# Kernel tuning notes

Hardware: AMD Instinct MI355X
Metric: run time of the kernel (lower is better)

Reference implementation:

```python
import jax, jax.numpy as jnp
import numpy as np

NUM_EMBEDDINGS = 8192
EMBEDDING_DIM = 64
COMMITMENT_COST = 0.25


def setup_inputs() -> dict:
    key = jax.random.key(0)
    k1, k2 = jax.random.split(key)
    hidden_states = jax.random.normal(k1, (32, 32, 32, EMBEDDING_DIM), dtype=jnp.float32)
    init_bound = 1.0 / NUM_EMBEDDINGS
    embedding = jax.random.uniform(k2, (NUM_EMBEDDINGS, EMBEDDING_DIM), dtype=jnp.float32,
                                   minval=-init_bound, maxval=init_bound)
    return {"hidden_states": hidden_states, "embedding": embedding}


def reference(hidden_states, embedding):
    # hidden_states: (B, H, W, D); embedding: (K, D)
    flat = hidden_states.reshape(-1, EMBEDDING_DIM)            # (N, D)
    z_sq = jnp.sum(flat * flat, axis=1, keepdims=True)          # (N, 1)
    e_sq = jnp.sum(embedding * embedding, axis=1)               # (K,)
    # squared L2 distances: ||z||^2 + ||e||^2 - 2 z.e
    distances = z_sq + e_sq - 2.0 * (flat @ embedding.T)        # (N, K)
    encoding_indices = jnp.argmin(distances, axis=1)            # (N,)
    # one-hot @ embedding == gather; identical math, efficient form
    quantized = jnp.take(embedding, encoding_indices, axis=0).reshape(hidden_states.shape)
    # codebook + commitment loss (return_loss=True path)
    loss = (jnp.mean((jax.lax.stop_gradient(quantized) - hidden_states) ** 2)
            + COMMITMENT_COST * jnp.mean((quantized - jax.lax.stop_gradient(hidden_states)) ** 2))
    # straight-through estimator
    z_q = hidden_states + jax.lax.stop_gradient(quantized - hidden_states)
    B = hidden_states.shape[0]
    min_encoding_indices = encoding_indices.reshape(B, -1)      # (B, num_tokens)
    return z_q, min_encoding_indices, loss
```

## Files before the change

### kernel.cpp

```cpp
#include <hip/hip_runtime.h>
#include <cfloat>

#define N_TOK   32768
#define DIM     64
#define K_CODES 8192
#define NCHK    64
#define TPB     128

#define IDX_OFF  (N_TOK * DIM)
#define LOSS_OFF (N_TOK * DIM + N_TOK)

#define WS_ESQ   0
#define WS_EHIT  8192
#define WS_PART  270336

#define W2_ESQ   0
#define W2_EHIT  8192
#define W2_ET    270336
#define W2_MM    794624
#define W2_PART  1843200
#define W2_TOTAL 1843456

#define MRG   2e-5f
#define DINIT 6e-5f

typedef __attribute__((ext_vector_type(8)))  short bf16x8;
typedef __attribute__((ext_vector_type(16))) float f32x16;

__device__ inline ushort f2bf(float x) {
    unsigned u = __float_as_uint(x);
    return (ushort)((u + 0x7FFFu + ((u >> 16) & 1u)) >> 16);
}
__device__ inline float bf2f(ushort h) { return __uint_as_float(((unsigned)h) << 16); }
__device__ inline ushort f2bf_up(float x) {
    unsigned u = __float_as_uint(x);
    return (x >= 0.0f) ? (ushort)((u + 0xFFFFu) >> 16) : (ushort)(u >> 16);
}
__device__ inline unsigned long long packdi(float d, int i) {
    unsigned u = __float_as_uint(d);
    u ^= (u & 0x80000000u) ? 0xFFFFFFFFu : 0x80000000u;
    return ((unsigned long long)u << 32) | (unsigned)i;
}

__global__ __launch_bounds__(256) void esq_kernel(const float* __restrict__ emb,
                                                  float* __restrict__ esq) {
#pragma clang fp contract(off)
    const int tid = threadIdx.x;
    const int q = tid & 7;
    const int code = blockIdx.x * 32 + (tid >> 3);
    const float* row = emb + code * DIM;
    float x = row[q];
    float r = x * x;
#pragma unroll
    for (int m = 1; m < 8; ++m) {
        float y = row[q + 8 * m];
        float sq = y * y;
        r = r + sq;
    }
    r = r + __shfl_xor(r, 1, 64);
    r = r + __shfl_xor(r, 2, 64);
    r = r + __shfl_xor(r, 4, 64);
    if (q == 0) esq[code] = r;
}

__global__ __launch_bounds__(256) void pack2(const float* __restrict__ emb,
                                             ushort* __restrict__ ehiT,
                                             float* __restrict__ eT) {
#pragma clang fp contract(off)
    const int k = blockIdx.x * 256 + threadIdx.x;
    float v[64];
    {
        const float4* ep = (const float4*)(emb + (size_t)k * DIM);
#pragma unroll
        for (int i = 0; i < 16; ++i) {
            const float4 a = ep[i];
            v[4 * i] = a.x; v[4 * i + 1] = a.y; v[4 * i + 2] = a.z; v[4 * i + 3] = a.w;
        }
    }
#pragma unroll
    for (int j = 0; j < 64; ++j) eT[(size_t)j * K_CODES + k] = v[j];
    const int sc = k >> 7, lc = k & 127;
#pragma unroll
    for (int q = 0; q < 4; ++q)
#pragma unroll
        for (int h = 0; h < 2; ++h) {
            bf16x8 o;
#pragma unroll
            for (int e = 0; e < 8; ++e) o[e] = (short)f2bf(v[16 * q + 8 * h + e]);
            *(bf16x8*)(ehiT + ((((size_t)sc * 4 + q) * 2 + h) * 128 + lc) * 8) = o;
        }
}

__global__ __launch_bounds__(256, 2) void vq_mfma(const float* __restrict__ hid,
                                                  const ushort* __restrict__ ehiT,
                                                  ushort* __restrict__ Mm) {
#pragma clang fp contract(off)
    const int tid = threadIdx.x;
    const int lane = tid & 63;
    const int w = tid >> 6;
    const int h = lane >> 5;
    const int t0 = blockIdx.x * 64;

    bf16x8 z_hi[2][4];
#pragma unroll
    for (int ts = 0; ts < 2; ++ts)
#pragma unroll
    for (int q = 0; q < 4; ++q) {
        const float* zp = hid + (size_t)(t0 + 32 * ts + (lane & 31)) * DIM + 16 * q + 8 * h;
        const float4 u0 = *(const float4*)zp;
        const float4 u1 = *(const float4*)(zp + 4);
        const float zz[8] = {u0.x, u0.y, u0.z, u0.w, u1.x, u1.y, u1.z, u1.w};
        bf16x8 hv;
#pragma unroll
        for (int i = 0; i < 8; ++i) hv[i] = (short)f2bf(zz[i]);
        z_hi[ts][q] = hv;
    }

    f32x16 zc;
#pragma unroll
    for (int i = 0; i < 16; ++i) zc[i] = 0.0f;

#define ALOAD(SC, R, Q) (*(const bf16x8*)(ehiT + \
    ((((size_t)(SC) * 4 + (Q)) * 2 + h) * 128 + 32 * (R) + (lane & 31)) * 8))

    bf16x8 Aa[4][4], Ab[4][4];
#pragma unroll
    for (int r = 0; r < 4; ++r)
#pragma unroll
        for (int q = 0; q < 4; ++q) Aa[r][q] = ALOAD(w, r, q);

#define MFMA_G(CUR, NXT, G) { \
    const int sc = 4 * (G) + w; \
    const int scn = ((G) + 1 < 16) ? (4 * ((G) + 1) + w) : sc; \
    _Pragma("unroll") \
    for (int r = 0; r < 4; ++r) \
        _Pragma("unroll") \
        for (int q = 0; q < 4; ++q) NXT[r][q] = ALOAD(scn, r, q); \
    float wm0 = -3.0e38f, wm1 = -3.0e38f; \
    _Pragma("unroll") \
    for (int r = 0; r < 4; ++r) { \
        f32x16 d0 = __builtin_amdgcn_mfma_f32_32x32x16_bf16(CUR[r][0], z_hi[0][0], zc, 0, 0, 0); \
        f32x16 d1 = __builtin_amdgcn_mfma_f32_32x32x16_bf16(CUR[r][0], z_hi[1][0], zc, 0, 0, 0); \
        _Pragma("unroll") \
        for (int q = 1; q < 4; ++q) { \
            d0 = __builtin_amdgcn_mfma_f32_32x32x16_bf16(CUR[r][q], z_hi[0][q], d0, 0, 0, 0); \
            d1 = __builtin_amdgcn_mfma_f32_32x32x16_bf16(CUR[r][q], z_hi[1][q], d1, 0, 0, 0); \
        } \
        _Pragma("unroll") \
        for (int i = 0; i < 16; ++i) { \
            wm0 = fmaxf(wm0, d0[i]); \
            wm1 = fmaxf(wm1, d1[i]); \
        } \
    } \
    wm0 = fmaxf(wm0, __shfl_xor(wm0, 32, 64)); \
    wm1 = fmaxf(wm1, __shfl_xor(wm1, 32, 64)); \
    if (lane < 32) { \
        Mm[(size_t)sc * N_TOK + t0 + lane]      = f2bf_up(wm0); \
        Mm[(size_t)sc * N_TOK + t0 + 32 + lane] = f2bf_up(wm1); \
    } }

    for (int gg = 0; gg < 16; gg += 2) {
        MFMA_G(Aa, Ab, gg)
        MFMA_G(Ab, Aa, gg + 1)
    }
#undef MFMA_G
#undef ALOAD
}

template <int FUSED>
__global__ __launch_bounds__(512, 1) void vq_select_t(const float* __restrict__ hid,
                                                      const float* __restrict__ eT,
                                                      const float* __restrict__ esq,
                                                      const ushort* __restrict__ Mm,
                                                      const float* __restrict__ emb,
                                                      float* __restrict__ out_zq,
                                                      float* __restrict__ out_idx,
                                                      float* __restrict__ partials) {
#pragma clang fp contract(off)
    __shared__ float z_s[TPB][68];
    __shared__ float zsq_s[TPB];
    __shared__ float eps_s[TPB];
    __shared__ float bD_s[TPB];
    __shared__ float mxw[4][TPB];
    __shared__ unsigned long long key_s[TPB];
    __shared__ unsigned long long m0_s[NCHK];
    __shared__ unsigned long long m1_s[NCHK];
    __shared__ float lred[2];

    const int tid = threadIdx.x;
    const int lane = tid & 63;
    const int w = tid >> 6;
    const int t0 = blockIdx.x * TPB;

    {
        const int t = tid >> 2;
        const int j4 = (tid & 3) * 4;
        const float4* src = (const float4*)(hid + (size_t)(t0 + t) * DIM);
        float4* dst = (float4*)(&z_s[t][0]);
#pragma unroll
        for (int i = 0; i < 4; ++i) dst[j4 + i] = src[j4 + i];
    }
    if (tid < TPB) key_s[tid] = ~0ull;
    __syncthreads();

    {
        const int token = tid & 127;
        const int cg = tid >> 7;
        float pm = bf2f(Mm[(size_t)(16 * cg) * N_TOK + t0 + token]);
#pragma unroll 5
        for (int c = 16 * cg + 1; c < 16 * cg + 16; ++c)
            pm = fmaxf(pm, bf2f(Mm[(size_t)c * N_TOK + t0 + token]));
        mxw[cg][token] = pm;
    }
    if (tid < TPB) {
        const float* zr = &z_s[tid][0];
        float r[8];
#pragma unroll
        for (int q = 0; q < 8; ++q) {
            float x = zr[q]; r[q] = x * x;
#pragma unroll
            for (int m = 1; m < 8; ++m) {
                float y = zr[q + 8 * m];
                float sq = y * y;
                r[q] = r[q] + sq;
            }
        }
        zsq_s[tid] = ((r[0] + r[1]) + (r[2] + r[3])) + ((r[4] + r[5]) + (r[6] + r[7]));
    }
    __syncthreads();
    if (tid < TPB) {
        const float mx = fmaxf(fmaxf(mxw[0][tid], mxw[1][tid]),
                               fmaxf(mxw[2][tid], mxw[3][tid]));
        const float zsq = zsq_s[tid];
        const float eps = sqrtf(zsq) * 4.2e-6f + 2e-7f;
        eps_s[tid] = eps;
        bD_s[tid] = zsq - 2.0f * mx + 2.0f * eps + DINIT;
    }
    __syncthreads();

#pragma unroll
    for (int i = 0; i < 8; ++i) {
        const int c = 8 * w + i;
        const float mA = bf2f(Mm[(size_t)c * N_TOK + t0 + lane]);
        const int sA = (fmaf(-2.0f, mA + eps_s[lane], zsq_s[lane]) - MRG) < bD_s[lane];
        const unsigned long long b0 = __ballot(sA);
        const float mB = bf2f(Mm[(size_t)c * N_TOK + t0 + 64 + lane]);
        const int sB = (fmaf(-2.0f, mB + eps_s[64 + lane], zsq_s[64 + lane]) - MRG) < bD_s[64 + lane];
        const unsigned long long b1 = __ballot(sB);
        if (lane == 0) { m0_s[c] = b0; m1_s[c] = b1; }
    }

    for (int i = 0; i < 8; ++i) {
        const int c = 8 * w + i;
        unsigned long long msk0 = m0_s[c], msk1 = m1_s[c];
        if (!(msk0 | msk1)) continue;
        const int k0 = c * 128 + 2 * lane;
        const float* eb = eT + k0;
        const float2 es2 = *(const float2*)(esq + k0);

        while (msk0 | msk1) {
            int G = 1;
            int tA, tB;
            if (msk0) { tA = __ffsll(msk0) - 1; msk0 &= msk0 - 1; }
            else      { tA = 64 + __ffsll(msk1) - 1; msk1 &= msk1 - 1; }
            tB = tA;
            if (msk0 | msk1) {
                G = 2;
                if (msk0) { tB = __ffsll(msk0) - 1; msk0 &= msk0 - 1; }
                else      { tB = 64 + __ffsll(msk1) - 1; msk1 &= msk1 - 1; }
            }
            const float4* zpA = (const float4*)(&z_s[tA][0]);
            const float4* zpB = (const float4*)(&z_s[tB][0]);

            float2 bA[8], bB[8];
            float aA0, aA1, aB0, aB1;
#define LOADG(B, G2) { _Pragma("unroll") \
    for (int j = 0; j < 8; ++j) \
        B[j] = *(const float2*)(eb + (size_t)(8 * (G2) + j) * K_CODES); }
#define FMAJ(Bj, vA, vB, COMP) \
    aA0 = fmaf(vA.COMP, Bj.x, aA0); aA1 = fmaf(vA.COMP, Bj.y, aA1); \
    aB0 = fmaf(vB.COMP, Bj.x, aB0); aB1 = fmaf(vB.COMP, Bj.y, aB1);
#define FMAG(B, G2) { \
    const float4 vA = zpA[2 * (G2)], vB = zpB[2 * (G2)]; \
    FMAJ(B[0], vA, vB, x) FMAJ(B[1], vA, vB, y) \
    FMAJ(B[2], vA, vB, z) FMAJ(B[3], vA, vB, w) \
    const float4 uA = zpA[2 * (G2) + 1], uB = zpB[2 * (G2) + 1]; \
    FMAJ(B[4], uA, uB, x) FMAJ(B[5], uA, uB, y) \
    FMAJ(B[6], uA, uB, z) FMAJ(B[7], uA, uB, w) }

            LOADG(bA, 0)
            LOADG(bB, 1)
            {
                const float4 vA = zpA[0], vB = zpB[0];
                aA0 = vA.x * bA[0].x; aA1 = vA.x * bA[0].y;
                aB0 = vB.x * bA[0].x; aB1 = vB.x * bA[0].y;
                FMAJ(bA[1], vA, vB, y)
                FMAJ(bA[2], vA, vB, z)
                FMAJ(bA[3], vA, vB, w)
                const float4 uA = zpA[1], uB = zpB[1];
                FMAJ(bA[4], uA, uB, x)
                FMAJ(bA[5], uA, uB, y)
                FMAJ(bA[6], uA, uB, z)
                FMAJ(bA[7], uA, uB, w)
            }
            LOADG(bA, 2) FMAG(bB, 1)
            LOADG(bB, 3) FMAG(bA, 2)
            LOADG(bA, 4) FMAG(bB, 3)
            LOADG(bB, 5) FMAG(bA, 4)
            LOADG(bA, 6) FMAG(bB, 5)
            LOADG(bB, 7) FMAG(bA, 6)
            FMAG(bB, 7)
#undef LOADG
#undef FMAJ
#undef FMAG

#define FINISH(aX0, aX1, tX) { \
    const float zqX = zsq_s[tX]; \
    const float dX0 = fmaf(-2.0f, aX0, zqX + es2.x); \
    const float dX1 = fmaf(-2.0f, aX1, zqX + es2.y); \
    float dl = dX0; int il = k0; \
    if (dX1 < dl) { dl = dX1; il = k0 + 1; } \
    _Pragma("unroll") \
    for (int mm = 1; mm < 64; mm <<= 1) { \
        const float ov = __shfl_xor(dl, mm, 64); \
        const int   oi = __shfl_xor(il, mm, 64); \
        if (ov < dl || (ov == dl && oi < il)) { dl = ov; il = oi; } \
    } \
    if (lane == 0) atomicMin(&key_s[tX], packdi(dl, il)); }

            FINISH(aA0, aA1, tA)
            if (G > 1) FINISH(aB0, aB1, tB)
#undef FINISH
        }
    }
    __syncthreads();

    if (FUSED) {
        if (tid < TPB) {
            const int t = t0 + tid;
            const int bi = (int)(key_s[tid] & 0xFFFFFFFFull);
            out_idx[t] = (float)bi;
            const float4* q4 = (const float4*)(emb + (size_t)bi * DIM);
            const float4* h4 = (const float4*)(&z_s[tid][0]);
            float4* o4 = (float4*)(out_zq + (size_t)t * DIM);
            float lsum = 0.f;
#pragma unroll
            for (int i = 0; i < 16; ++i) {
                const float4 q = q4[i];
                const float4 h = h4[i];
                float4 zq;
                float dx;
                dx = q.x - h.x; zq.x = h.x + dx; lsum += dx * dx;
                dx = q.y - h.y; zq.y = h.y + dx; lsum += dx * dx;
                dx = q.z - h.z; zq.z = h.z + dx; lsum += dx * dx;
                dx = q.w - h.w; zq.w = h.w + dx; lsum += dx * dx;
                o4[i] = zq;
            }
#pragma unroll
            for (int off = 32; off >= 1; off >>= 1) lsum += __shfl_xor(lsum, off, 64);
            if ((tid & 63) == 0) lred[tid >> 6] = lsum;
        }
        __syncthreads();
        if (tid == 0) partials[blockIdx.x] = lred[0] + lred[1];
    } else {
        if (tid < TPB) out_idx[t0 + tid] = (float)(int)(key_s[tid] & 0xFFFFFFFFull);
    }
}

__global__ __launch_bounds__(256) void vq_finish(const float* __restrict__ hid,
                                                 const float* __restrict__ emb,
                                                 const float* __restrict__ out_idx,
                                                 float* __restrict__ out_zq,
                                                 float* __restrict__ partials) {
#pragma clang fp contract(off)
    __shared__ float lred[4];
    const int tid = threadIdx.x;
    const int t = blockIdx.x * 256 + tid;

    const int bi = (int)out_idx[t];

    const float4* q4 = (const float4*)(emb + (size_t)bi * DIM);
    const float4* h4 = (const float4*)(hid + (size_t)t * DIM);
    float4* o4 = (float4*)(out_zq + (size_t)t * DIM);
    float lsum = 0.f;
#pragma unroll
    for (int i = 0; i < 16; ++i) {
        const float4 q = q4[i];
        const float4 h = h4[i];
        float4 zq;
        float dx;
        dx = q.x - h.x; zq.x = h.x + dx; lsum += dx * dx;
        dx = q.y - h.y; zq.y = h.y + dx; lsum += dx * dx;
        dx = q.z - h.z; zq.z = h.z + dx; lsum += dx * dx;
        dx = q.w - h.w; zq.w = h.w + dx; lsum += dx * dx;
        o4[i] = zq;
    }

#pragma unroll
    for (int off = 32; off >= 1; off >>= 1) lsum += __shfl_xor(lsum, off, 64);
    const int wid = tid >> 6;
    if ((tid & 63) == 0) lred[wid] = lsum;
    __syncthreads();
    if (tid == 0) partials[blockIdx.x] = (lred[0] + lred[1]) + (lred[2] + lred[3]);
}

__global__ __launch_bounds__(128) void loss_kernel128(const float* __restrict__ partials,
                                                      float* __restrict__ out_loss) {
#pragma clang fp contract(off)
    __shared__ float s[128];
    const int t = threadIdx.x;
    s[t] = partials[t];
    __syncthreads();
    for (int off = 64; off >= 1; off >>= 1) {
        if (t < off) s[t] = s[t] + s[t + off];
        __syncthreads();
    }
    if (t == 0) {
        const float m = s[0] * (1.0f / 2097152.0f);
        out_loss[0] = m + 0.25f * m;
    }
}

__global__ __launch_bounds__(128) void loss_kernel256(const float* __restrict__ partials,
                                                      float* __restrict__ out_loss) {
#pragma clang fp contract(off)
    __shared__ float s[128];
    const int t = threadIdx.x;
    s[t] = partials[t] + partials[t + 128];
    __syncthreads();
    for (int off = 64; off >= 1; off >>= 1) {
        if (t < off) s[t] = s[t] + s[t + off];
        __syncthreads();
    }
    if (t == 0) {
        const float m = s[0] * (1.0f / 2097152.0f);
        out_loss[0] = m + 0.25f * m;
    }
}

extern "C" void kernel_launch(void* const* d_in, const int* in_sizes, int n_in,
                              void* d_out, int out_size, void* d_ws, size_t ws_size,
                              hipStream_t stream) {
    const float* hid = (const float*)d_in[0];
    const float* emb = (const float*)d_in[1];
    float* out = (float*)d_out;
    float* ws  = (float*)d_ws;

    if (ws_size >= (size_t)W2_TOTAL * sizeof(float)) {
        float*  esq   = ws + W2_ESQ;
        ushort* ehiT  = (ushort*)(ws + W2_EHIT);
        float*  eT    = ws + W2_ET;
        ushort* Mm    = (ushort*)(ws + W2_MM);
        float*  parts = ws + W2_PART;

        esq_kernel<<<K_CODES / 32, 256, 0, stream>>>(emb, esq);
        pack2<<<K_CODES / 256, 256, 0, stream>>>(emb, ehiT, eT);
        vq_mfma<<<N_TOK / 64, 256, 0, stream>>>(hid, ehiT, Mm);
        vq_select_t<1><<<N_TOK / TPB, 512, 0, stream>>>(hid, eT, esq, Mm, emb,
                                                        out, out + IDX_OFF, parts);
        loss_kernel256<<<1, 128, 0, stream>>>(parts, out + LOSS_OFF);
    } else {
        float*  esq   = ws + WS_ESQ;
        ushort* ehiT  = (ushort*)(ws + WS_EHIT);
        float*  parts = ws + WS_PART;
        float*  eT    = out;
        ushort* Mm    = (ushort*)(out + 524288);

        esq_kernel<<<K_CODES / 32, 256, 0, stream>>>(emb, esq);
        pack2<<<K_CODES / 256, 256, 0, stream>>>(emb, ehiT, eT);
        vq_mfma<<<N_TOK / 64, 256, 0, stream>>>(hid, ehiT, Mm);
        vq_select_t<0><<<N_TOK / TPB, 512, 0, stream>>>(hid, eT, esq, Mm, emb,
                                                        out, out + IDX_OFF, parts);
        vq_finish<<<N_TOK / 256, 256, 0, stream>>>(hid, emb, out + IDX_OFF, out, parts);
        loss_kernel128<<<1, 128, 0, stream>>>(parts, out + LOSS_OFF);
    }
}
```

Baseline: 132.4 us.

## Evaluate best-bound chunk first to tighten pruning threshold before candidate scan

The select kernel now records which 128-code chunk has the highest bf16 upper-bound score per token and evaluates that chunk exactly first. The exact best distance found there replaces the heuristic bound (zsq - 2*max + slack) as the pruning threshold for the remaining chunks, so fewer chunks pass the filter and need exact FP32 dot products. It adds an extra pass with two more block barriers, and it serializes the first-chunk evaluation before the main scan.

```diff
diff --git a/kernel.cpp b/kernel.cpp
--- a/kernel.cpp
+++ b/kernel.cpp
@@ -22,7 +22,6 @@
 #define W2_TOTAL 1843456
 
 #define MRG   2e-5f
-#define DINIT 6e-5f
 
 typedef __attribute__((ext_vector_type(8)))  short bf16x8;
 typedef __attribute__((ext_vector_type(16))) float f32x16;
@@ -40,6 +39,11 @@
     unsigned u = __float_as_uint(d);
     u ^= (u & 0x80000000u) ? 0xFFFFFFFFu : 0x80000000u;
     return ((unsigned long long)u << 32) | (unsigned)i;
+}
+__device__ inline float unpackd(unsigned long long k) {
+    unsigned u = (unsigned)(k >> 32);
+    u = (u & 0x80000000u) ? (u ^ 0x80000000u) : ~u;
+    return __uint_as_float(u);
 }
 
 __global__ __launch_bounds__(256) void esq_kernel(const float* __restrict__ emb,
@@ -167,113 +171,37 @@
 #undef ALOAD
 }
 
-template <int FUSED>
-__global__ __launch_bounds__(512, 1) void vq_select_t(const float* __restrict__ hid,
-                                                      const float* __restrict__ eT,
-                                                      const float* __restrict__ esq,
-                                                      const ushort* __restrict__ Mm,
-                                                      const float* __restrict__ emb,
-                                                      float* __restrict__ out_zq,
-                                                      float* __restrict__ out_idx,
-                                                      float* __restrict__ partials) {
-#pragma clang fp contract(off)
-    __shared__ float z_s[TPB][68];
-    __shared__ float zsq_s[TPB];
-    __shared__ float eps_s[TPB];
-    __shared__ float bD_s[TPB];
-    __shared__ float mxw[4][TPB];
-    __shared__ unsigned long long key_s[TPB];
-    __shared__ unsigned long long m0_s[NCHK];
-    __shared__ unsigned long long m1_s[NCHK];
-    __shared__ float lred[2];
-
-    const int tid = threadIdx.x;
-    const int lane = tid & 63;
-    const int w = tid >> 6;
-    const int t0 = blockIdx.x * TPB;
-
-    {
-        const int t = tid >> 2;
-        const int j4 = (tid & 3) * 4;
-        const float4* src = (const float4*)(hid + (size_t)(t0 + t) * DIM);
-        float4* dst = (float4*)(&z_s[t][0]);
-#pragma unroll
-        for (int i = 0; i < 4; ++i) dst[j4 + i] = src[j4 + i];
-    }
-    if (tid < TPB) key_s[tid] = ~0ull;
-    __syncthreads();
-
-    {
-        const int token = tid & 127;
-        const int cg = tid >> 7;
-        float pm = bf2f(Mm[(size_t)(16 * cg) * N_TOK + t0 + token]);
-#pragma unroll 5
-        for (int c = 16 * cg + 1; c < 16 * cg + 16; ++c)
-            pm = fmaxf(pm, bf2f(Mm[(size_t)c * N_TOK + t0 + token]));
-        mxw[cg][token] = pm;
-    }
-    if (tid < TPB) {
-        const float* zr = &z_s[tid][0];
-        float r[8];
-#pragma unroll
-        for (int q = 0; q < 8; ++q) {
-            float x = zr[q]; r[q] = x * x;
-#pragma unroll
-            for (int m = 1; m < 8; ++m) {
-                float y = zr[q + 8 * m];
-                float sq = y * y;
-                r[q] = r[q] + sq;
-            }
-        }
-        zsq_s[tid] = ((r[0] + r[1]) + (r[2] + r[3])) + ((r[4] + r[5]) + (r[6] + r[7]));
-    }
-    __syncthreads();
-    if (tid < TPB) {
-        const float mx = fmaxf(fmaxf(mxw[0][tid], mxw[1][tid]),
-                               fmaxf(mxw[2][tid], mxw[3][tid]));
-        const float zsq = zsq_s[tid];
-        const float eps = sqrtf(zsq) * 4.2e-6f + 2e-7f;
-        eps_s[tid] = eps;
-        bD_s[tid] = zsq - 2.0f * mx + 2.0f * eps + DINIT;
-    }
-    __syncthreads();
-
-#pragma unroll
-    for (int i = 0; i < 8; ++i) {
-        const int c = 8 * w + i;
-        const float mA = bf2f(Mm[(size_t)c * N_TOK + t0 + lane]);
-        const int sA = (fmaf(-2.0f, mA + eps_s[lane], zsq_s[lane]) - MRG) < bD_s[lane];
-        const unsigned long long b0 = __ballot(sA);
-        const float mB = bf2f(Mm[(size_t)c * N_TOK + t0 + 64 + lane]);
-        const int sB = (fmaf(-2.0f, mB + eps_s[64 + lane], zsq_s[64 + lane]) - MRG) < bD_s[64 + lane];
-        const unsigned long long b1 = __ballot(sB);
-        if (lane == 0) { m0_s[c] = b0; m1_s[c] = b1; }
-    }
-
-    for (int i = 0; i < 8; ++i) {
-        const int c = 8 * w + i;
-        unsigned long long msk0 = m0_s[c], msk1 = m1_s[c];
-        if (!(msk0 | msk1)) continue;
-        const int k0 = c * 128 + 2 * lane;
-        const float* eb = eT + k0;
-        const float2 es2 = *(const float2*)(esq + k0);
-
-        while (msk0 | msk1) {
-            int G = 1;
-            int tA, tB;
-            if (msk0) { tA = __ffsll(msk0) - 1; msk0 &= msk0 - 1; }
-            else      { tA = 64 + __ffsll(msk1) - 1; msk1 &= msk1 - 1; }
-            tB = tA;
-            if (msk0 | msk1) {
-                G = 2;
-                if (msk0) { tB = __ffsll(msk0) - 1; msk0 &= msk0 - 1; }
-                else      { tB = 64 + __ffsll(msk1) - 1; msk1 &= msk1 - 1; }
-            }
-            const float4* zpA = (const float4*)(&z_s[tA][0]);
-            const float4* zpB = (const float4*)(&z_s[tB][0]);
-
-            float2 bA[8], bB[8];
-            float aA0, aA1, aB0, aB1;
+__device__ __forceinline__ void eval_chunk(const int c,
+                                           unsigned long long msk0,
+                                           unsigned long long msk1,
+                                           const float* __restrict__ eT,
+                                           const float* __restrict__ esq,
+                                           const float (*z_s)[68],
+                                           const float* zsq_s,
+                                           unsigned long long* key_s,
+                                           const int lane) {
+#pragma clang fp contract(off)
+    if (!(msk0 | msk1)) return;
+    const int k0 = c * 128 + 2 * lane;
+    const float* eb = eT + k0;
+    const float2 es2 = *(const float2*)(esq + k0);
+
+    while (msk0 | msk1) {
+        int G = 1;
+        int tA, tB;
+        if (msk0) { tA = __ffsll(msk0) - 1; msk0 &= msk0 - 1; }
+        else      { tA = 64 + __ffsll(msk1) - 1; msk1 &= msk1 - 1; }
+        tB = tA;
+        if (msk0 | msk1) {
+            G = 2;
+            if (msk0) { tB = __ffsll(msk0) - 1; msk0 &= msk0 - 1; }
+            else      { tB = 64 + __ffsll(msk1) - 1; msk1 &= msk1 - 1; }
+        }
+        const float4* zpA = (const float4*)(&z_s[tA][0]);
+        const float4* zpB = (const float4*)(&z_s[tB][0]);
+
+        float2 bA[8], bB[8];
+        float aA0, aA1, aB0, aB1;
 #define LOADG(B, G2) { _Pragma("unroll") \
     for (int j = 0; j < 8; ++j) \
         B[j] = *(const float2*)(eb + (size_t)(8 * (G2) + j) * K_CODES); }
@@ -288,28 +216,28 @@
     FMAJ(B[4], uA, uB, x) FMAJ(B[5], uA, uB, y) \
     FMAJ(B[6], uA, uB, z) FMAJ(B[7], uA, uB, w) }
 
-            LOADG(bA, 0)
-            LOADG(bB, 1)
-            {
-                const float4 vA = zpA[0], vB = zpB[0];
-                aA0 = vA.x * bA[0].x; aA1 = vA.x * bA[0].y;
-                aB0 = vB.x * bA[0].x; aB1 = vB.x * bA[0].y;
-                FMAJ(bA[1], vA, vB, y)
-                FMAJ(bA[2], vA, vB, z)
-                FMAJ(bA[3], vA, vB, w)
-                const float4 uA = zpA[1], uB = zpB[1];
-                FMAJ(bA[4], uA, uB, x)
-                FMAJ(bA[5], uA, uB, y)
-                FMAJ(bA[6], uA, uB, z)
-                FMAJ(bA[7], uA, uB, w)
-            }
-            LOADG(bA, 2) FMAG(bB, 1)
-            LOADG(bB, 3) FMAG(bA, 2)
-            LOADG(bA, 4) FMAG(bB, 3)
-            LOADG(bB, 5) FMAG(bA, 4)
-            LOADG(bA, 6) FMAG(bB, 5)
-            LOADG(bB, 7) FMAG(bA, 6)
-            FMAG(bB, 7)
+        LOADG(bA, 0)
+        LOADG(bB, 1)
+        {
+            const float4 vA = zpA[0], vB = zpB[0];
+            aA0 = vA.x * bA[0].x; aA1 = vA.x * bA[0].y;
+            aB0 = vB.x * bA[0].x; aB1 = vB.x * bA[0].y;
+            FMAJ(bA[1], vA, vB, y)
+            FMAJ(bA[2], vA, vB, z)
+            FMAJ(bA[3], vA, vB, w)
+            const float4 uA = zpA[1], uB = zpB[1];
+            FMAJ(bA[4], uA, uB, x)
+            FMAJ(bA[5], uA, uB, y)
+            FMAJ(bA[6], uA, uB, z)
+            FMAJ(bA[7], uA, uB, w)
+        }
+        LOADG(bA, 2) FMAG(bB, 1)
+        LOADG(bB, 3) FMAG(bA, 2)
+        LOADG(bA, 4) FMAG(bB, 3)
+        LOADG(bB, 5) FMAG(bA, 4)
+        LOADG(bA, 6) FMAG(bB, 5)
+        LOADG(bB, 7) FMAG(bA, 6)
+        FMAG(bB, 7)
 #undef LOADG
 #undef FMAJ
 #undef FMAG
@@ -328,10 +256,109 @@
     } \
     if (lane == 0) atomicMin(&key_s[tX], packdi(dl, il)); }
 
-            FINISH(aA0, aA1, tA)
-            if (G > 1) FINISH(aB0, aB1, tB)
+        FINISH(aA0, aA1, tA)
+        if (G > 1) FINISH(aB0, aB1, tB)
 #undef FINISH
-        }
+    }
+}
+
+template <int FUSED>
+__global__ __launch_bounds__(512, 1) void vq_select_t(const float* __restrict__ hid,
+                                                      const float* __restrict__ eT,
+                                                      const float* __restrict__ esq,
+                                                      const ushort* __restrict__ Mm,
+                                                      const float* __restrict__ emb,
+                                                      float* __restrict__ out_zq,
+                                                      float* __restrict__ out_idx,
+                                                      float* __restrict__ partials) {
+#pragma clang fp contract(off)
+    __shared__ float z_s[TPB][68];
+    __shared__ float zsq_s[TPB];
+    __shared__ float eps_s[TPB];
+    __shared__ float bD_s[TPB];
+    __shared__ float mxw[4][TPB];
+    __shared__ int   cw[4][TPB];
+    __shared__ int   cstar_s[TPB];
+    __shared__ unsigned long long key_s[TPB];
+    __shared__ float lred[2];
+
+    const int tid = threadIdx.x;
+    const int lane = tid & 63;
+    const int w = tid >> 6;
+    const int t0 = blockIdx.x * TPB;
+
+    {
+        const int t = tid >> 2;
+        const int j4 = (tid & 3) * 4;
+        const float4* src = (const float4*)(hid + (size_t)(t0 + t) * DIM);
+        float4* dst = (float4*)(&z_s[t][0]);
+#pragma unroll
+        for (int i = 0; i < 4; ++i) dst[j4 + i] = src[j4 + i];
+    }
+    if (tid < TPB) key_s[tid] = ~0ull;
+    __syncthreads();
+
+    {
+        const int token = tid & 127;
+        const int cg = tid >> 7;
+        const int c0 = 16 * cg;
+        float pm = bf2f(Mm[(size_t)c0 * N_TOK + t0 + token]);
+        int   pc = c0;
+#pragma unroll 5
+        for (int c = c0 + 1; c < c0 + 16; ++c) {
+            const float v = bf2f(Mm[(size_t)c * N_TOK + t0 + token]);
+            if (v > pm) { pm = v; pc = c; }
+        }
+        mxw[cg][token] = pm;
+        cw[cg][token] = pc;
+    }
+    if (tid < TPB) {
+        const float* zr = &z_s[tid][0];
+        float r[8];
+#pragma unroll
+        for (int q = 0; q < 8; ++q) {
+            float x = zr[q]; r[q] = x * x;
+#pragma unroll
+            for (int m = 1; m < 8; ++m) {
+                float y = zr[q + 8 * m];
+                float sq = y * y;
+                r[q] = r[q] + sq;
+            }
+        }
+        zsq_s[tid] = ((r[0] + r[1]) + (r[2] + r[3])) + ((r[4] + r[5]) + (r[6] + r[7]));
+    }
+    __syncthreads();
+    if (tid < TPB) {
+        float mx = mxw[0][tid]; int cst = cw[0][tid];
+#pragma unroll
+        for (int g = 1; g < 4; ++g)
+            if (mxw[g][tid] > mx) { mx = mxw[g][tid]; cst = cw[g][tid]; }
+        cstar_s[tid] = cst;
+        eps_s[tid] = sqrtf(zsq_s[tid]) * 4.2e-6f + 2e-7f;
+    }
+    __syncthreads();
+
+    for (int i = 0; i < 8; ++i) {
+        const int c = 8 * w + i;
+        const unsigned long long m0 = __ballot(cstar_s[lane] == c);
+        const unsigned long long m1 = __ballot(cstar_s[64 + lane] == c);
+        eval_chunk(c, m0, m1, eT, esq, z_s, zsq_s, key_s, lane);
+    }
+    __syncthreads();
+    if (tid < TPB) bD_s[tid] = unpackd(key_s[tid]);
+    __syncthreads();
+
+    for (int i = 0; i < 8; ++i) {
+        const int c = 8 * w + i;
+        const float mA = bf2f(Mm[(size_t)c * N_TOK + t0 + lane]);
+        const int sA = ((fmaf(-2.0f, mA + eps_s[lane], zsq_s[lane]) - MRG) < bD_s[lane])
+                       && (cstar_s[lane] != c);
+        const unsigned long long m0 = __ballot(sA);
+        const float mB = bf2f(Mm[(size_t)c * N_TOK + t0 + 64 + lane]);
+        const int sB = ((fmaf(-2.0f, mB + eps_s[64 + lane], zsq_s[64 + lane]) - MRG) < bD_s[64 + lane])
+                       && (cstar_s[64 + lane] != c);
+        const unsigned long long m1 = __ballot(sB);
+        eval_chunk(c, m0, m1, eT, esq, z_s, zsq_s, key_s, lane);
     }
     __syncthreads();
 
```

New measurement: 136.6 us. 1.03x slower.

## Halve codebook chunk size to 64 codes for finer candidate pruning

Applied to the files above, without the earlier changes.

The MFMA pass now records a bf16 upper-bound max per 64-code chunk instead of per 128-code chunk, doubling the chunk-max table. The select kernel marks and exactly evaluates candidate chunks at this finer granularity, with each lane handling one code instead of two. The aim is fewer fp32 exact dot products on chunks that cannot hold the argmin. The cost is twice the Mm writes and reads, more ballot and mask passes, and half as many codes per exact-evaluation iteration. Workspace offsets are adjusted to fit the larger table.

```diff
diff --git a/kernel.cpp b/kernel.cpp
--- a/kernel.cpp
+++ b/kernel.cpp
@@ -4,7 +4,7 @@
 #define N_TOK   32768
 #define DIM     64
 #define K_CODES 8192
-#define NCHK    64
+#define NCHK    128
 #define TPB     128
 
 #define IDX_OFF  (N_TOK * DIM)
@@ -12,14 +12,15 @@
 
 #define WS_ESQ   0
 #define WS_EHIT  8192
-#define WS_PART  270336
+#define WS_ET    270336
+#define WS_PART  794624
 
 #define W2_ESQ   0
 #define W2_EHIT  8192
 #define W2_ET    270336
 #define W2_MM    794624
-#define W2_PART  1843200
-#define W2_TOTAL 1843456
+#define W2_PART  2891776
+#define W2_TOTAL 2892032
 
 #define MRG   2e-5f
 #define DINIT 6e-5f
@@ -129,16 +130,9 @@
 #pragma unroll
         for (int q = 0; q < 4; ++q) Aa[r][q] = ALOAD(w, r, q);
 
-#define MFMA_G(CUR, NXT, G) { \
-    const int sc = 4 * (G) + w; \
-    const int scn = ((G) + 1 < 16) ? (4 * ((G) + 1) + w) : sc; \
+#define MFMA_HALF(CUR, R0, WM0, WM1) { \
     _Pragma("unroll") \
-    for (int r = 0; r < 4; ++r) \
-        _Pragma("unroll") \
-        for (int q = 0; q < 4; ++q) NXT[r][q] = ALOAD(scn, r, q); \
-    float wm0 = -3.0e38f, wm1 = -3.0e38f; \
-    _Pragma("unroll") \
-    for (int r = 0; r < 4; ++r) { \
+    for (int r = (R0); r < (R0) + 2; ++r) { \
         f32x16 d0 = __builtin_amdgcn_mfma_f32_32x32x16_bf16(CUR[r][0], z_hi[0][0], zc, 0, 0, 0); \
         f32x16 d1 = __builtin_amdgcn_mfma_f32_32x32x16_bf16(CUR[r][0], z_hi[1][0], zc, 0, 0, 0); \
         _Pragma("unroll") \
@@ -148,15 +142,30 @@
         } \
         _Pragma("unroll") \
         for (int i = 0; i < 16; ++i) { \
-            wm0 = fmaxf(wm0, d0[i]); \
-            wm1 = fmaxf(wm1, d1[i]); \
+            WM0 = fmaxf(WM0, d0[i]); \
+            WM1 = fmaxf(WM1, d1[i]); \
         } \
-    } \
-    wm0 = fmaxf(wm0, __shfl_xor(wm0, 32, 64)); \
-    wm1 = fmaxf(wm1, __shfl_xor(wm1, 32, 64)); \
+    } }
+
+#define MFMA_G(CUR, NXT, G) { \
+    const int sc = 4 * (G) + w; \
+    const int scn = ((G) + 1 < 16) ? (4 * ((G) + 1) + w) : sc; \
+    _Pragma("unroll") \
+    for (int r = 0; r < 4; ++r) \
+        _Pragma("unroll") \
+        for (int q = 0; q < 4; ++q) NXT[r][q] = ALOAD(scn, r, q); \
+    float wma0 = -3.0e38f, wma1 = -3.0e38f, wmb0 = -3.0e38f, wmb1 = -3.0e38f; \
+    MFMA_HALF(CUR, 0, wma0, wma1) \
+    MFMA_HALF(CUR, 2, wmb0, wmb1) \
+    wma0 = fmaxf(wma0, __shfl_xor(wma0, 32, 64)); \
+    wma1 = fmaxf(wma1, __shfl_xor(wma1, 32, 64)); \
+    wmb0 = fmaxf(wmb0, __shfl_xor(wmb0, 32, 64)); \
+    wmb1 = fmaxf(wmb1, __shfl_xor(wmb1, 32, 64)); \
     if (lane < 32) { \
-        Mm[(size_t)sc * N_TOK + t0 + lane]      = f2bf_up(wm0); \
-        Mm[(size_t)sc * N_TOK + t0 + 32 + lane] = f2bf_up(wm1); \
+        Mm[(size_t)(2 * sc) * N_TOK + t0 + lane]          = f2bf_up(wma0); \
+        Mm[(size_t)(2 * sc) * N_TOK + t0 + 32 + lane]     = f2bf_up(wma1); \
+        Mm[(size_t)(2 * sc + 1) * N_TOK + t0 + lane]      = f2bf_up(wmb0); \
+        Mm[(size_t)(2 * sc + 1) * N_TOK + t0 + 32 + lane] = f2bf_up(wmb1); \
     } }
 
     for (int gg = 0; gg < 16; gg += 2) {
@@ -164,7 +173,95 @@
         MFMA_G(Ab, Aa, gg + 1)
     }
 #undef MFMA_G
+#undef MFMA_HALF
 #undef ALOAD
+}
+
+__device__ __forceinline__ void eval_chunk64(const int c,
+                                             unsigned long long msk0,
+                                             unsigned long long msk1,
+                                             const float* __restrict__ eT,
+                                             const float* __restrict__ esq,
+                                             const float (*z_s)[68],
+                                             const float* zsq_s,
+                                             unsigned long long* key_s,
+                                             const int lane) {
+#pragma clang fp contract(off)
+    if (!(msk0 | msk1)) return;
+    const int k0 = c * 64 + lane;
+    const float* eb = eT + k0;
+    const float es1 = esq[k0];
+
+    while (msk0 | msk1) {
+        int G = 1;
+        int tA, tB;
+        if (msk0) { tA = __ffsll(msk0) - 1; msk0 &= msk0 - 1; }
+        else      { tA = 64 + __ffsll(msk1) - 1; msk1 &= msk1 - 1; }
+        tB = tA;
+        if (msk0 | msk1) {
+            G = 2;
+            if (msk0) { tB = __ffsll(msk0) - 1; msk0 &= msk0 - 1; }
+            else      { tB = 64 + __ffsll(msk1) - 1; msk1 &= msk1 - 1; }
+        }
+        const float4* zpA = (const float4*)(&z_s[tA][0]);
+        const float4* zpB = (const float4*)(&z_s[tB][0]);
+
+        float bA[8], bB[8];
+        float aA0, aB0;
+#define LOADG(B, G2) { _Pragma("unroll") \
+    for (int j = 0; j < 8; ++j) \
+        B[j] = eb[(size_t)(8 * (G2) + j) * K_CODES]; }
+#define FMAG(B, G2) { \
+    const float4 vA = zpA[2 * (G2)], vB = zpB[2 * (G2)]; \
+    aA0 = fmaf(vA.x, B[0], aA0); aB0 = fmaf(vB.x, B[0], aB0); \
+    aA0 = fmaf(vA.y, B[1], aA0); aB0 = fmaf(vB.y, B[1], aB0); \
+    aA0 = fmaf(vA.z, B[2], aA0); aB0 = fmaf(vB.z, B[2], aB0); \
+    aA0 = fmaf(vA.w, B[3], aA0); aB0 = fmaf(vB.w, B[3], aB0); \
+    const float4 uA = zpA[2 * (G2) + 1], uB = zpB[2 * (G2) + 1]; \
+    aA0 = fmaf(uA.x, B[4], aA0); aB0 = fmaf(uB.x, B[4], aB0); \
+    aA0 = fmaf(uA.y, B[5], aA0); aB0 = fmaf(uB.y, B[5], aB0); \
+    aA0 = fmaf(uA.z, B[6], aA0); aB0 = fmaf(uB.z, B[6], aB0); \
+    aA0 = fmaf(uA.w, B[7], aA0); aB0 = fmaf(uB.w, B[7], aB0); }
+
+        LOADG(bA, 0)
+        LOADG(bB, 1)
+        {
+            const float4 vA = zpA[0], vB = zpB[0];
+            aA0 = vA.x * bA[0]; aB0 = vB.x * bA[0];
+            aA0 = fmaf(vA.y, bA[1], aA0); aB0 = fmaf(vB.y, bA[1], aB0);
+            aA0 = fmaf(vA.z, bA[2], aA0); aB0 = fmaf(vB.z, bA[2], aB0);
+            aA0 = fmaf(vA.w, bA[3], aA0); aB0 = fmaf(vB.w, bA[3], aB0);
+            const float4 uA = zpA[1], uB = zpB[1];
+            aA0 = fmaf(uA.x, bA[4], aA0); aB0 = fmaf(uB.x, bA[4], aB0);
+            aA0 = fmaf(uA.y, bA[5], aA0); aB0 = fmaf(uB.y, bA[5], aB0);
+            aA0 = fmaf(uA.z, bA[6], aA0); aB0 = fmaf(uB.z, bA[6], aB0);
+            aA0 = fmaf(uA.w, bA[7], aA0); aB0 = fmaf(uB.w, bA[7], aB0);
+        }
+        LOADG(bA, 2) FMAG(bB, 1)
+        LOADG(bB, 3) FMAG(bA, 2)
+        LOADG(bA, 4) FMAG(bB, 3)
+        LOADG(bB, 5) FMAG(bA, 4)
+        LOADG(bA, 6) FMAG(bB, 5)
+        LOADG(bB, 7) FMAG(bA, 6)
+        FMAG(bB, 7)
+#undef LOADG
+#undef FMAG
+
+#define FINISH(aX0, tX) { \
+    float dl = fmaf(-2.0f, aX0, zsq_s[tX] + es1); \
+    int il = k0; \
+    _Pragma("unroll") \
+    for (int mm = 1; mm < 64; mm <<= 1) { \
+        const float ov = __shfl_xor(dl, mm, 64); \
+        const int   oi = __shfl_xor(il, mm, 64); \
+        if (ov < dl || (ov == dl && oi < il)) { dl = ov; il = oi; } \
+    } \
+    if (lane == 0) atomicMin(&key_s[tX], packdi(dl, il)); }
+
+        FINISH(aA0, tA)
+        if (G > 1) FINISH(aB0, tB)
+#undef FINISH
+    }
 }
 
 template <int FUSED>
@@ -206,9 +303,10 @@
     {
         const int token = tid & 127;
         const int cg = tid >> 7;
-        float pm = bf2f(Mm[(size_t)(16 * cg) * N_TOK + t0 + token]);
-#pragma unroll 5
-        for (int c = 16 * cg + 1; c < 16 * cg + 16; ++c)
+        const int c0 = 32 * cg;
+        float pm = bf2f(Mm[(size_t)c0 * N_TOK + t0 + token]);
+#pragma unroll 8
+        for (int c = c0 + 1; c < c0 + 32; ++c)
             pm = fmaxf(pm, bf2f(Mm[(size_t)c * N_TOK + t0 + token]));
         mxw[cg][token] = pm;
     }
@@ -239,8 +337,8 @@
     __syncthreads();
 
 #pragma unroll
-    for (int i = 0; i < 8; ++i) {
-        const int c = 8 * w + i;
+    for (int i = 0; i < 16; ++i) {
+        const int c = 16 * w + i;
         const float mA = bf2f(Mm[(size_t)c * N_TOK + t0 + lane]);
         const int sA = (fmaf(-2.0f, mA + eps_s[lane], zsq_s[lane]) - MRG) < bD_s[lane];
         const unsigned long long b0 = __ballot(sA);
@@ -250,88 +348,9 @@
         if (lane == 0) { m0_s[c] = b0; m1_s[c] = b1; }
     }
 
-    for (int i = 0; i < 8; ++i) {
-        const int c = 8 * w + i;
-        unsigned long long msk0 = m0_s[c], msk1 = m1_s[c];
-        if (!(msk0 | msk1)) continue;
-        const int k0 = c * 128 + 2 * lane;
-        const float* eb = eT + k0;
-        const float2 es2 = *(const float2*)(esq + k0);
-
-        while (msk0 | msk1) {
-            int G = 1;
-            int tA, tB;
-            if (msk0) { tA = __ffsll(msk0) - 1; msk0 &= msk0 - 1; }
-            else      { tA = 64 + __ffsll(msk1) - 1; msk1 &= msk1 - 1; }
-            tB = tA;
-            if (msk0 | msk1) {
-                G = 2;
-                if (msk0) { tB = __ffsll(msk0) - 1; msk0 &= msk0 - 1; }
-                else      { tB = 64 + __ffsll(msk1) - 1; msk1 &= msk1 - 1; }
-            }
-            const float4* zpA = (const float4*)(&z_s[tA][0]);
-            const float4* zpB = (const float4*)(&z_s[tB][0]);
-
-            float2 bA[8], bB[8];
-            float aA0, aA1, aB0, aB1;
-#define LOADG(B, G2) { _Pragma("unroll") \
-    for (int j = 0; j < 8; ++j) \
-        B[j] = *(const float2*)(eb + (size_t)(8 * (G2) + j) * K_CODES); }
-#define FMAJ(Bj, vA, vB, COMP) \
-    aA0 = fmaf(vA.COMP, Bj.x, aA0); aA1 = fmaf(vA.COMP, Bj.y, aA1); \
-    aB0 = fmaf(vB.COMP, Bj.x, aB0); aB1 = fmaf(vB.COMP, Bj.y, aB1);
-#define FMAG(B, G2) { \
-    const float4 vA = zpA[2 * (G2)], vB = zpB[2 * (G2)]; \
-    FMAJ(B[0], vA, vB, x) FMAJ(B[1], vA, vB, y) \
-    FMAJ(B[2], vA, vB, z) FMAJ(B[3], vA, vB, w) \
-    const float4 uA = zpA[2 * (G2) + 1], uB = zpB[2 * (G2) + 1]; \
-    FMAJ(B[4], uA, uB, x) FMAJ(B[5], uA, uB, y) \
-    FMAJ(B[6], uA, uB, z) FMAJ(B[7], uA, uB, w) }
-
-            LOADG(bA, 0)
-            LOADG(bB, 1)
-            {
-                const float4 vA = zpA[0], vB = zpB[0];
-                aA0 = vA.x * bA[0].x; aA1 = vA.x * bA[0].y;
-                aB0 = vB.x * bA[0].x; aB1 = vB.x * bA[0].y;
-                FMAJ(bA[1], vA, vB, y)
-                FMAJ(bA[2], vA, vB, z)
-                FMAJ(bA[3], vA, vB, w)
-                const float4 uA = zpA[1], uB = zpB[1];
-                FMAJ(bA[4], uA, uB, x)
-                FMAJ(bA[5], uA, uB, y)
-                FMAJ(bA[6], uA, uB, z)
-                FMAJ(bA[7], uA, uB, w)
-            }
-            LOADG(bA, 2) FMAG(bB, 1)
-            LOADG(bB, 3) FMAG(bA, 2)
-            LOADG(bA, 4) FMAG(bB, 3)
-            LOADG(bB, 5) FMAG(bA, 4)
-            LOADG(bA, 6) FMAG(bB, 5)
-            LOADG(bB, 7) FMAG(bA, 6)
-            FMAG(bB, 7)
-#undef LOADG
-#undef FMAJ
-#undef FMAG
-
-#define FINISH(aX0, aX1, tX) { \
-    const float zqX = zsq_s[tX]; \
-    const float dX0 = fmaf(-2.0f, aX0, zqX + es2.x); \
-    const float dX1 = fmaf(-2.0f, aX1, zqX + es2.y); \
-    float dl = dX0; int il = k0; \
-    if (dX1 < dl) { dl = dX1; il = k0 + 1; } \
-    _Pragma("unroll") \
-    for (int mm = 1; mm < 64; mm <<= 1) { \
-        const float ov = __shfl_xor(dl, mm, 64); \
-        const int   oi = __shfl_xor(il, mm, 64); \
-        if (ov < dl || (ov == dl && oi < il)) { dl = ov; il = oi; } \
-    } \
-    if (lane == 0) atomicMin(&key_s[tX], packdi(dl, il)); }
-
-            FINISH(aA0, aA1, tA)
-            if (G > 1) FINISH(aB0, aB1, tB)
-#undef FINISH
-        }
+    for (int i = 0; i < 16; ++i) {
+        const int c = 16 * w + i;
+        eval_chunk64(c, m0_s[c], m1_s[c], eT, esq, z_s, zsq_s, key_s, lane);
     }
     __syncthreads();
 
@@ -462,9 +481,9 @@
     } else {
         float*  esq   = ws + WS_ESQ;
         ushort* ehiT  = (ushort*)(ws + WS_EHIT);
+        float*  eT    = ws + WS_ET;
         float*  parts = ws + WS_PART;
-        float*  eT    = out;
-        ushort* Mm    = (ushort*)(out + 524288);
+        ushort* Mm    = (ushort*)out;
 
         esq_kernel<<<K_CODES / 32, 256, 0, stream>>>(emb, esq);
         pack2<<<K_CODES / 256, 256, 0, stream>>>(emb, ehiT, eT);
```

Result: faster. 128.6 us (-2.9%).
